# Optimization experiments

Measured on AMD Instinct MI355X. Metric: run time of the kernel, lower is better.

The kernel has to match this reference:

```python
import jax, jax.numpy as jnp
import numpy as np

B, L, D, K, V = 256, 50, 128, 4, 50000
LENGTH = 5      # opt.length
BETA = 0.01     # opt.beta scaling on loss1
EPS = 1e-12     # F.normalize eps


def _l2norm(x, axis):
    n = jnp.sqrt(jnp.sum(x * x, axis=axis, keepdims=True))
    return x / jnp.maximum(n, EPS)


def setup_inputs() -> dict:
    key = jax.random.key(0)
    ks = jax.random.split(key, 11)
    s = 1.0 / np.sqrt(D)  # reset_parameters: uniform(-stdv, stdv)
    u = lambda k, shape: jax.random.uniform(k, shape, jnp.float32, -s, s)
    return {
        "hidden": jax.random.normal(ks[0], (B, L, D), jnp.float32),
        "mask": jnp.ones((B, L), jnp.int32),
        "pos_emb": u(ks[1], (L, D)),
        "w1": u(ks[2], (2 * D, D)),
        "w2": u(ks[3], (D, K)),
        "glu1_w": u(ks[4], (D, K * D)),
        "glu1_b": u(ks[5], (K * D,)),
        "att_w1": u(ks[6], (D, D)),
        "att_w2": u(ks[7], (D, D)),
        "att_v": u(ks[8], (D, K)),
        "emb": u(ks[9], (V, D)),
    }


def reference(hidden, mask, pos_emb, w1, w2, glu1_w, glu1_b, att_w1, att_w2, att_v, emb):
    m = mask.astype(jnp.float32)[..., None]                       # [B,L,1]
    hs = jnp.sum(hidden * m, axis=1) / jnp.sum(m, axis=1)         # [B,D] masked mean
    # nh = tanh(cat(pos, hidden) @ w1); then sigmoid(glu1)
    cat = jnp.concatenate([jnp.broadcast_to(pos_emb[None], hidden.shape), hidden], axis=-1)
    nh = jnp.tanh(cat @ w1)                                       # [B,L,D]
    nh = jax.nn.sigmoid(nh @ glu1_w + glu1_b)                     # [B,L,K*D]
    # torch.split(dim=2) + stack(dim=3) -> [B,L,D,K]
    nh = nh.reshape(B, L, K, D).transpose(0, 1, 3, 2)             # [B,L,D,K]
    beta = jnp.einsum('bldk,dk->blk', nh, w2)                     # [B,L,K]
    # attention gate alpha = sigmoid(att_v(tanh(W1 hs + W2 hidden)))
    att = jnp.tanh(hs[:, None, :] @ att_w1 + hidden @ att_w2)     # [B,L,D]
    alpha = jax.nn.sigmoid(att @ att_v)                           # [B,L,K]
    beta = beta * (0.5 + alpha) * m                               # mask over interests
    # per-interest L2 normalize along sequence (fused over K)
    nb = _l2norm(beta, axis=1)                                    # [B,L,K]
    # pairwise |cos| between interests: vectorized Gram instead of python loops
    G = jnp.einsum('bli,blj->bij', nb, nb)                        # [B,K,K]
    triu = jnp.triu(jnp.ones((K, K), jnp.float32), 1)
    sim = jnp.sum(jnp.abs(G) * triu, axis=(1, 2)) * (2.0 / (K * (K - 1)))  # [B]
    lens = jnp.sum(mask, axis=1).astype(jnp.float32) - LENGTH     # sumask[:,0] - length
    loss1 = jnp.sum(jax.nn.sigmoid(sim * lens))                   # scalar
    # per-interest pooled session reps, stacked on leading axis -> [K,B,D]
    select = jnp.einsum('blk,bld->kbd', beta, hidden)
    b_norm = _l2norm(emb[1:], axis=-1)                            # [V-1,D]
    scores = jnp.einsum('kbd,vd->kbv', select, b_norm)            # [K,B,V-1]
    max_scores = jnp.max(scores, axis=0)                          # [B,V-1]
    return (max_scores, loss1 * BETA, scores)
```

## Files before the change

kernel.cpp:

```cpp
#include <hip/hip_runtime.h>
#include <hip/hip_bf16.h>
#include <math.h>

constexpr int NB = 256;
constexpr int NL = 50;
constexpr int ND = 128;
constexpr int NK = 4;
constexpr int NVOC = 50000;
constexpr int NVm1 = 49999;
constexpr int NPAD = 50048;
constexpr int ROWS = NB * NL;
constexpr int MROWS = NB * NK;

typedef __bf16 bf16x8 __attribute__((ext_vector_type(8)));
typedef float f32x4 __attribute__((ext_vector_type(4)));

__device__ __forceinline__ float sigm_fast(float x) { return 1.0f / (1.0f + __expf(-x)); }
__device__ __forceinline__ float sigm_prec(float x) { return 1.0f / (1.0f + expf(-x)); }

__global__ void k_hs_lens(const float* __restrict__ hidden, const int* __restrict__ mask,
                          float* __restrict__ hs, float* __restrict__ lens) {
    int b = blockIdx.x;
    int d = threadIdx.x;
    float acc = 0.f, msum = 0.f;
    for (int l = 0; l < NL; ++l) {
        float mv = (float)mask[b * NL + l];
        acc += hidden[((size_t)b * NL + l) * ND + d] * mv;
        msum += mv;
    }
    hs[b * ND + d] = acc / msum;
    if (d == 0) lens[b] = msum - 5.0f;
}

__global__ void k_rowmat(const float* __restrict__ rows, const float* __restrict__ mat,
                         float* __restrict__ outp) {
    int r = blockIdx.x;
    int d = threadIdx.x;
    __shared__ float s[ND];
    s[d] = rows[r * ND + d];
    __syncthreads();
    float acc = 0.f;
#pragma unroll 8
    for (int j = 0; j < ND; ++j) acc += s[j] * mat[j * ND + d];
    outp[r * ND + d] = acc;
}

__global__ __launch_bounds__(256) void k_nh_att(
    const float* __restrict__ hidden, const float* __restrict__ w1,
    const float* __restrict__ att_w2, const float* __restrict__ att_v,
    const float* __restrict__ posPart, const float* __restrict__ hsW1,
    float* __restrict__ nh_out, float* __restrict__ alpha_out) {
    constexpr int R = 32;
    __shared__ float X[R * ND];
    __shared__ float ATT[R * 132];
    int row0 = blockIdx.x * R;
    int tid = threadIdx.x;
    for (int i = tid; i < R * ND; i += 256) X[i] = hidden[(size_t)row0 * ND + i];
    __syncthreads();
    int d = tid & 127;
    int rg = tid >> 7;
    float accN[16], accA[16];
#pragma unroll
    for (int r = 0; r < 16; ++r) { accN[r] = 0.f; accA[r] = 0.f; }
    for (int j = 0; j < ND; ++j) {
        float w1v = w1[(ND + j) * ND + d];
        float awv = att_w2[j * ND + d];
#pragma unroll
        for (int r = 0; r < 16; ++r) {
            float x = X[(rg * 16 + r) * ND + j];
            accN[r] += x * w1v;
            accA[r] += x * awv;
        }
    }
#pragma unroll
    for (int r = 0; r < 16; ++r) {
        int row = row0 + rg * 16 + r;
        int b = row / NL;
        int l = row - b * NL;
        float nhv = tanhf(posPart[l * ND + d] + accN[r]);
        float atv = tanhf(hsW1[b * ND + d] + accA[r]);
        nh_out[(size_t)row * ND + d] = nhv;
        ATT[(rg * 16 + r) * 132 + d] = atv;
    }
    __syncthreads();
    if (tid < 128) {
        int rl = tid >> 2;
        int k = tid & 3;
        float acc = 0.f;
        for (int dd = 0; dd < ND; ++dd) acc += ATT[rl * 132 + dd] * att_v[dd * NK + k];
        alpha_out[(size_t)(row0 + rl) * NK + k] = sigm_fast(acc);
    }
}

__global__ __launch_bounds__(256) void k_glu_beta(
    const float* __restrict__ nh, const float* __restrict__ glu1_w,
    const float* __restrict__ glu1_b, const float* __restrict__ w2,
    const float* __restrict__ alpha, const int* __restrict__ mask,
    float* __restrict__ beta_out) {
    constexpr int R = 16;
    __shared__ float NHs[R * ND];
    __shared__ float P[R * 513];
    int row0 = blockIdx.x * R;
    int tid = threadIdx.x;
    for (int i = tid; i < R * ND; i += 256) NHs[i] = nh[(size_t)row0 * ND + i];
    __syncthreads();
    float acc0[R], acc1[R];
#pragma unroll
    for (int r = 0; r < R; ++r) { acc0[r] = 0.f; acc1[r] = 0.f; }
    int c0 = tid, c1 = tid + 256;
    for (int j = 0; j < ND; ++j) {
        float g0 = glu1_w[j * 512 + c0];
        float g1 = glu1_w[j * 512 + c1];
#pragma unroll
        for (int r = 0; r < R; ++r) {
            float x = NHs[r * ND + j];
            acc0[r] += x * g0;
            acc1[r] += x * g1;
        }
    }
    float bb0 = glu1_b[c0], bb1 = glu1_b[c1];
    float w20 = w2[(c0 & 127) * NK + (c0 >> 7)];
    float w21 = w2[(c1 & 127) * NK + (c1 >> 7)];
#pragma unroll
    for (int r = 0; r < R; ++r) {
        P[r * 513 + c0] = sigm_fast(acc0[r] + bb0) * w20;
        P[r * 513 + c1] = sigm_fast(acc1[r] + bb1) * w21;
    }
    __syncthreads();
    if (tid < 64) {
        int r = tid >> 2;
        int k = tid & 3;
        float s = 0.f;
        for (int dd = 0; dd < ND; ++dd) s += P[r * 513 + k * ND + dd];
        int row = row0 + r;
        float mv = (float)mask[row];
        float a = alpha[(size_t)row * NK + k];
        beta_out[(size_t)row * NK + k] = s * (0.5f + a) * mv;
    }
}

__global__ void k_loss_b(const float* __restrict__ beta, const float* __restrict__ lens,
                         float* __restrict__ lossb) {
    int b = blockIdx.x;
    int t = threadIdx.x;
    float bk[NK] = {0.f, 0.f, 0.f, 0.f};
    if (t < NL) {
#pragma unroll
        for (int k = 0; k < NK; ++k) bk[k] = beta[((size_t)b * NL + t) * NK + k];
    }
    float nb[NK];
#pragma unroll
    for (int k = 0; k < NK; ++k) {
        float v = bk[k] * bk[k];
        for (int off = 32; off >= 1; off >>= 1) v += __shfl_xor(v, off);
        nb[k] = bk[k] / fmaxf(sqrtf(v), 1e-12f);
    }
    float sim = 0.f;
#pragma unroll
    for (int i = 0; i < NK; ++i) {
#pragma unroll
        for (int j = 0; j < NK; ++j) {
            if (j > i) {
                float p = nb[i] * nb[j];
                for (int off = 32; off >= 1; off >>= 1) p += __shfl_xor(p, off);
                sim += fabsf(p);
            }
        }
    }
    sim *= (2.0f / (NK * (NK - 1)));
    if (t == 0) lossb[b] = sigm_prec(sim * lens[b]);
}

__global__ void k_loss_red(const float* __restrict__ lossb, float* __restrict__ out_scalar) {
    __shared__ float red[4];
    int t = threadIdx.x;
    float v = lossb[t];
    for (int off = 32; off >= 1; off >>= 1) v += __shfl_xor(v, off);
    if ((t & 63) == 0) red[t >> 6] = v;
    __syncthreads();
    if (t == 0) out_scalar[0] = (red[0] + red[1] + red[2] + red[3]) * 0.01f;
}

__global__ void k_select(const float* __restrict__ beta, const float* __restrict__ hidden,
                         __hip_bfloat16* __restrict__ selb) {
    int b = blockIdx.x;
    int d = threadIdx.x;
    float acc[NK] = {0.f, 0.f, 0.f, 0.f};
    for (int l = 0; l < NL; ++l) {
        float h = hidden[((size_t)b * NL + l) * ND + d];
        const float* bp = &beta[((size_t)b * NL + l) * NK];
        acc[0] += bp[0] * h;
        acc[1] += bp[1] * h;
        acc[2] += bp[2] * h;
        acc[3] += bp[3] * h;
    }
#pragma unroll
    for (int k = 0; k < NK; ++k)
        selb[((size_t)b * NK + k) * ND + d] = __float2bfloat16(acc[k]);
}

__global__ void k_bnorm(const float* __restrict__ emb, __hip_bfloat16* __restrict__ bn) {
    int v = blockIdx.x * 2 + (threadIdx.x >> 7);
    int j = threadIdx.x & 127;
    __shared__ float red[4];
    float x = 0.f;
    if (v < NVm1) x = emb[((size_t)v + 1) * ND + j];
    float ss = x * x;
    for (int off = 32; off >= 1; off >>= 1) ss += __shfl_xor(ss, off);
    int w = threadIdx.x >> 6;
    if ((threadIdx.x & 63) == 0) red[w] = ss;
    __syncthreads();
    float tot = (threadIdx.x < 128) ? (red[0] + red[1]) : (red[2] + red[3]);
    float rn = 1.f / fmaxf(sqrtf(tot), 1e-12f);
    bn[(size_t)v * ND + j] = __float2bfloat16(x * rn);
}

__global__ __launch_bounds__(256) void k_gemm(
    const __hip_bfloat16* __restrict__ selb, const __hip_bfloat16* __restrict__ bn,
    float* __restrict__ scores, float* __restrict__ maxs) {
    int bn0 = blockIdx.x * 128;
    int bm0 = blockIdx.y * 128;
    int wave = threadIdx.x >> 6;
    int lane = threadIdx.x & 63;
    int l16 = lane & 15;
    int quad = lane >> 4;
    int m_off = bm0 + (wave >> 1) * 64;
    int n_off = bn0 + (wave & 1) * 64;

    f32x4 acc[4][4];
#pragma unroll
    for (int mi = 0; mi < 4; ++mi)
#pragma unroll
        for (int ni = 0; ni < 4; ++ni) acc[mi][ni] = (f32x4){0.f, 0.f, 0.f, 0.f};

    const bf16x8* A = reinterpret_cast<const bf16x8*>(selb);
    const bf16x8* Bv = reinterpret_cast<const bf16x8*>(bn);
#pragma unroll
    for (int kk = 0; kk < 4; ++kk) {
        int koff = kk * 4 + quad;
        bf16x8 afr[4], bfr[4];
#pragma unroll
        for (int mi = 0; mi < 4; ++mi)
            afr[mi] = A[(size_t)(m_off + mi * 16 + l16) * 16 + koff];
#pragma unroll
        for (int ni = 0; ni < 4; ++ni)
            bfr[ni] = Bv[(size_t)(n_off + ni * 16 + l16) * 16 + koff];
#pragma unroll
        for (int mi = 0; mi < 4; ++mi)
#pragma unroll
            for (int ni = 0; ni < 4; ++ni)
                acc[mi][ni] = __builtin_amdgcn_mfma_f32_16x16x32_bf16(
                    afr[mi], bfr[ni], acc[mi][ni], 0, 0, 0);
    }

#pragma unroll
    for (int mi = 0; mi < 4; ++mi) {
        int m_base = m_off + mi * 16;
        int bidx = (m_base >> 2) + quad;
#pragma unroll
        for (int ni = 0; ni < 4; ++ni) {
            int n = n_off + ni * 16 + l16;
            if (n < NVm1) {
                float mx = acc[mi][ni][0];
#pragma unroll
                for (int r = 0; r < 4; ++r) {
                    float val = acc[mi][ni][r];
                    scores[(size_t)r * NB * NVm1 + (size_t)bidx * NVm1 + n] = val;
                    mx = fmaxf(mx, val);
                }
                maxs[(size_t)bidx * NVm1 + n] = mx;
            }
        }
    }
}

extern "C" void kernel_launch(void* const* d_in, const int* in_sizes, int n_in,
                              void* d_out, int out_size, void* d_ws, size_t ws_size,
                              hipStream_t stream) {
    const float* hidden  = (const float*)d_in[0];
    const int*   mask    = (const int*)d_in[1];
    const float* pos_emb = (const float*)d_in[2];
    const float* w1      = (const float*)d_in[3];
    const float* w2      = (const float*)d_in[4];
    const float* glu1_w  = (const float*)d_in[5];
    const float* glu1_b  = (const float*)d_in[6];
    const float* att_w1  = (const float*)d_in[7];
    const float* att_w2  = (const float*)d_in[8];
    const float* att_v   = (const float*)d_in[9];
    const float* emb     = (const float*)d_in[10];

    float* out      = (float*)d_out;
    float* max_out  = out;
    float* loss_out = out + (size_t)NB * NVm1;
    float* scores   = out + (size_t)NB * NVm1 + 1;

    char* w = (char*)d_ws;
    auto alloc = [&](size_t bytes) {
        char* p = w;
        w += (bytes + 255) & ~(size_t)255;
        return p;
    };
    float* posPart = (float*)alloc((size_t)NL * ND * 4);
    float* hs      = (float*)alloc((size_t)NB * ND * 4);
    float* lensv   = (float*)alloc((size_t)NB * 4);
    float* hsW1    = (float*)alloc((size_t)NB * ND * 4);
    float* nh      = (float*)alloc((size_t)ROWS * ND * 4);
    float* alphav  = (float*)alloc((size_t)ROWS * NK * 4);
    float* betav   = (float*)alloc((size_t)ROWS * NK * 4);
    float* lossb   = (float*)alloc((size_t)NB * 4);
    __hip_bfloat16* selb = (__hip_bfloat16*)alloc((size_t)MROWS * ND * 2);
    __hip_bfloat16* bnv  = (__hip_bfloat16*)alloc((size_t)NPAD * ND * 2);

    k_hs_lens<<<NB, 128, 0, stream>>>(hidden, mask, hs, lensv);
    k_rowmat<<<NL, 128, 0, stream>>>(pos_emb, w1, posPart);
    k_rowmat<<<NB, 128, 0, stream>>>(hs, att_w1, hsW1);
    k_nh_att<<<ROWS / 32, 256, 0, stream>>>(hidden, w1, att_w2, att_v, posPart, hsW1, nh, alphav);
    k_glu_beta<<<ROWS / 16, 256, 0, stream>>>(nh, glu1_w, glu1_b, w2, alphav, mask, betav);
    k_loss_b<<<NB, 64, 0, stream>>>(betav, lensv, lossb);
    k_loss_red<<<1, 256, 0, stream>>>(lossb, loss_out);
    k_select<<<NB, 128, 0, stream>>>(betav, hidden, selb);
    k_bnorm<<<NPAD / 2, 256, 0, stream>>>(emb, bnv);
    k_gemm<<<dim3(NPAD / 128, MROWS / 128), 256, 0, stream>>>(selb, bnv, scores, max_out);
}
```

Measured before the change: 516.8 us.

## Fuse small kernels, vectorize matmul inner loops, stage GEMM tiles in LDS

Merges several small launches: the two row-matmuls become one kernel, select and bnorm share one kernel, and the loss reduction becomes an atomicAdd inside the per-batch loss kernel, which now computes lens itself. The inner loops of nh/att and glu are rewritten to read float4 from shared memory with explicit FMA chains. The GEMM now loads A and B tiles into LDS via global_load_lds with an XOR swizzle and loops over four N tiles per block, reusing the A tile. This trades fewer launches and better operand reuse for more LDS and synchronization. The atomic loss sum makes the accumulation order nondeterministic.

```diff
diff --git a/kernel.cpp b/kernel.cpp
--- a/kernel.cpp
+++ b/kernel.cpp
@@ -6,11 +6,11 @@
 constexpr int NL = 50;
 constexpr int ND = 128;
 constexpr int NK = 4;
-constexpr int NVOC = 50000;
 constexpr int NVm1 = 49999;
-constexpr int NPAD = 50048;
+constexpr int NPAD2 = 50176;
 constexpr int ROWS = NB * NL;
 constexpr int MROWS = NB * NK;
+constexpr int GEMM_NT = 4;
 
 typedef __bf16 bf16x8 __attribute__((ext_vector_type(8)));
 typedef float f32x4 __attribute__((ext_vector_type(4)));
@@ -18,8 +18,14 @@
 __device__ __forceinline__ float sigm_fast(float x) { return 1.0f / (1.0f + __expf(-x)); }
 __device__ __forceinline__ float sigm_prec(float x) { return 1.0f / (1.0f + expf(-x)); }
 
-__global__ void k_hs_lens(const float* __restrict__ hidden, const int* __restrict__ mask,
-                          float* __restrict__ hs, float* __restrict__ lens) {
+__device__ __forceinline__ void gld_lds16(const void* g, void* l) {
+    __builtin_amdgcn_global_load_lds(
+        (const __attribute__((address_space(1))) void*)g,
+        (__attribute__((address_space(3))) void*)l, 16, 0, 0);
+}
+
+__global__ void k_hs(const float* __restrict__ hidden, const int* __restrict__ mask,
+                     float* __restrict__ hs, float* __restrict__ loss_out) {
     int b = blockIdx.x;
     int d = threadIdx.x;
     float acc = 0.f, msum = 0.f;
@@ -29,20 +35,25 @@
         msum += mv;
     }
     hs[b * ND + d] = acc / msum;
-    if (d == 0) lens[b] = msum - 5.0f;
-}
-
-__global__ void k_rowmat(const float* __restrict__ rows, const float* __restrict__ mat,
-                         float* __restrict__ outp) {
+    if (b == 0 && d == 0) loss_out[0] = 0.f;
+}
+
+__global__ void k_rowmats(const float* __restrict__ pos_emb, const float* __restrict__ w1,
+                          const float* __restrict__ hs, const float* __restrict__ att_w1,
+                          float* __restrict__ posPart, float* __restrict__ hsW1) {
     int r = blockIdx.x;
     int d = threadIdx.x;
+    const float *src, *mat;
+    float* dst;
+    if (r < NL) { src = pos_emb + (size_t)r * ND; mat = w1;     dst = posPart + (size_t)r * ND; }
+    else        { int b = r - NL; src = hs + (size_t)b * ND; mat = att_w1; dst = hsW1 + (size_t)b * ND; }
     __shared__ float s[ND];
-    s[d] = rows[r * ND + d];
+    s[d] = src[d];
     __syncthreads();
     float acc = 0.f;
 #pragma unroll 8
     for (int j = 0; j < ND; ++j) acc += s[j] * mat[j * ND + d];
-    outp[r * ND + d] = acc;
+    dst[d] = acc;
 }
 
 __global__ __launch_bounds__(256) void k_nh_att(
@@ -62,14 +73,20 @@
     float accN[16], accA[16];
 #pragma unroll
     for (int r = 0; r < 16; ++r) { accN[r] = 0.f; accA[r] = 0.f; }
-    for (int j = 0; j < ND; ++j) {
-        float w1v = w1[(ND + j) * ND + d];
-        float awv = att_w2[j * ND + d];
+    const float4* Xv = (const float4*)X;
+    for (int j4 = 0; j4 < 32; ++j4) {
+        float w1v[4], awv[4];
+#pragma unroll
+        for (int u = 0; u < 4; ++u) {
+            int j = j4 * 4 + u;
+            w1v[u] = w1[(ND + j) * ND + d];
+            awv[u] = att_w2[j * ND + d];
+        }
 #pragma unroll
         for (int r = 0; r < 16; ++r) {
-            float x = X[(rg * 16 + r) * ND + j];
-            accN[r] += x * w1v;
-            accA[r] += x * awv;
+            float4 xv = Xv[(rg * 16 + r) * 32 + j4];
+            accN[r] = fmaf(xv.w, w1v[3], fmaf(xv.z, w1v[2], fmaf(xv.y, w1v[1], fmaf(xv.x, w1v[0], accN[r]))));
+            accA[r] = fmaf(xv.w, awv[3], fmaf(xv.z, awv[2], fmaf(xv.y, awv[1], fmaf(xv.x, awv[0], accA[r]))));
         }
     }
 #pragma unroll
@@ -108,14 +125,20 @@
 #pragma unroll
     for (int r = 0; r < R; ++r) { acc0[r] = 0.f; acc1[r] = 0.f; }
     int c0 = tid, c1 = tid + 256;
-    for (int j = 0; j < ND; ++j) {
-        float g0 = glu1_w[j * 512 + c0];
-        float g1 = glu1_w[j * 512 + c1];
+    const float4* Nv = (const float4*)NHs;
+    for (int j4 = 0; j4 < 32; ++j4) {
+        float g0v[4], g1v[4];
+#pragma unroll
+        for (int u = 0; u < 4; ++u) {
+            int j = j4 * 4 + u;
+            g0v[u] = glu1_w[j * 512 + c0];
+            g1v[u] = glu1_w[j * 512 + c1];
+        }
 #pragma unroll
         for (int r = 0; r < R; ++r) {
-            float x = NHs[r * ND + j];
-            acc0[r] += x * g0;
-            acc1[r] += x * g1;
+            float4 xv = Nv[r * 32 + j4];
+            acc0[r] = fmaf(xv.w, g0v[3], fmaf(xv.z, g0v[2], fmaf(xv.y, g0v[1], fmaf(xv.x, g0v[0], acc0[r]))));
+            acc1[r] = fmaf(xv.w, g1v[3], fmaf(xv.z, g1v[2], fmaf(xv.y, g1v[1], fmaf(xv.x, g1v[0], acc1[r]))));
         }
     }
     float bb0 = glu1_b[c0], bb1 = glu1_b[c1];
@@ -139,10 +162,14 @@
     }
 }
 
-__global__ void k_loss_b(const float* __restrict__ beta, const float* __restrict__ lens,
-                         float* __restrict__ lossb) {
+__global__ void k_loss(const float* __restrict__ beta, const int* __restrict__ mask,
+                       float* __restrict__ loss_out) {
     int b = blockIdx.x;
     int t = threadIdx.x;
+    float mv = (t < NL) ? (float)mask[b * NL + t] : 0.f;
+    float msum = mv;
+    for (int off = 32; off >= 1; off >>= 1) msum += __shfl_xor(msum, off);
+    float lens = msum - 5.0f;
     float bk[NK] = {0.f, 0.f, 0.f, 0.f};
     if (t < NL) {
 #pragma unroll
@@ -168,109 +195,135 @@
         }
     }
     sim *= (2.0f / (NK * (NK - 1)));
-    if (t == 0) lossb[b] = sigm_prec(sim * lens[b]);
-}
-
-__global__ void k_loss_red(const float* __restrict__ lossb, float* __restrict__ out_scalar) {
-    __shared__ float red[4];
-    int t = threadIdx.x;
-    float v = lossb[t];
-    for (int off = 32; off >= 1; off >>= 1) v += __shfl_xor(v, off);
-    if ((t & 63) == 0) red[t >> 6] = v;
-    __syncthreads();
-    if (t == 0) out_scalar[0] = (red[0] + red[1] + red[2] + red[3]) * 0.01f;
-}
-
-__global__ void k_select(const float* __restrict__ beta, const float* __restrict__ hidden,
-                         __hip_bfloat16* __restrict__ selb) {
-    int b = blockIdx.x;
-    int d = threadIdx.x;
-    float acc[NK] = {0.f, 0.f, 0.f, 0.f};
-    for (int l = 0; l < NL; ++l) {
-        float h = hidden[((size_t)b * NL + l) * ND + d];
-        const float* bp = &beta[((size_t)b * NL + l) * NK];
-        acc[0] += bp[0] * h;
-        acc[1] += bp[1] * h;
-        acc[2] += bp[2] * h;
-        acc[3] += bp[3] * h;
-    }
-#pragma unroll
-    for (int k = 0; k < NK; ++k)
-        selb[((size_t)b * NK + k) * ND + d] = __float2bfloat16(acc[k]);
-}
-
-__global__ void k_bnorm(const float* __restrict__ emb, __hip_bfloat16* __restrict__ bn) {
-    int v = blockIdx.x * 2 + (threadIdx.x >> 7);
-    int j = threadIdx.x & 127;
-    __shared__ float red[4];
-    float x = 0.f;
-    if (v < NVm1) x = emb[((size_t)v + 1) * ND + j];
-    float ss = x * x;
-    for (int off = 32; off >= 1; off >>= 1) ss += __shfl_xor(ss, off);
-    int w = threadIdx.x >> 6;
-    if ((threadIdx.x & 63) == 0) red[w] = ss;
-    __syncthreads();
-    float tot = (threadIdx.x < 128) ? (red[0] + red[1]) : (red[2] + red[3]);
-    float rn = 1.f / fmaxf(sqrtf(tot), 1e-12f);
-    bn[(size_t)v * ND + j] = __float2bfloat16(x * rn);
+    if (t == 0) atomicAdd(loss_out, sigm_prec(sim * lens) * 0.01f);
+}
+
+__global__ __launch_bounds__(256) void k_sel_bnorm(
+    const float* __restrict__ beta, const float* __restrict__ hidden,
+    const float* __restrict__ emb, __hip_bfloat16* __restrict__ selb,
+    __hip_bfloat16* __restrict__ bnv) {
+    int blk = blockIdx.x;
+    int tid = threadIdx.x;
+    if (blk < NPAD2 / 2) {
+        int v = blk * 2 + (tid >> 7);
+        int j = tid & 127;
+        __shared__ float red[4];
+        float x = 0.f;
+        if (v < NVm1) x = emb[((size_t)v + 1) * ND + j];
+        float ss = x * x;
+        for (int off = 32; off >= 1; off >>= 1) ss += __shfl_xor(ss, off);
+        int w = tid >> 6;
+        if ((tid & 63) == 0) red[w] = ss;
+        __syncthreads();
+        float tot = (tid < 128) ? (red[0] + red[1]) : (red[2] + red[3]);
+        float rn = 1.f / fmaxf(sqrtf(tot), 1e-12f);
+        bnv[(size_t)v * ND + j] = __float2bfloat16(x * rn);
+    } else {
+        int b = (blk - NPAD2 / 2) * 2 + (tid >> 7);
+        int d = tid & 127;
+        float a0 = 0.f, a1 = 0.f, a2 = 0.f, a3 = 0.f;
+        for (int l = 0; l < NL; ++l) {
+            float h = hidden[((size_t)b * NL + l) * ND + d];
+            const float* bp = &beta[((size_t)b * NL + l) * NK];
+            a0 = fmaf(bp[0], h, a0);
+            a1 = fmaf(bp[1], h, a1);
+            a2 = fmaf(bp[2], h, a2);
+            a3 = fmaf(bp[3], h, a3);
+        }
+        selb[((size_t)b * NK + 0) * ND + d] = __float2bfloat16(a0);
+        selb[((size_t)b * NK + 1) * ND + d] = __float2bfloat16(a1);
+        selb[((size_t)b * NK + 2) * ND + d] = __float2bfloat16(a2);
+        selb[((size_t)b * NK + 3) * ND + d] = __float2bfloat16(a3);
+    }
 }
 
 __global__ __launch_bounds__(256) void k_gemm(
     const __hip_bfloat16* __restrict__ selb, const __hip_bfloat16* __restrict__ bn,
     float* __restrict__ scores, float* __restrict__ maxs) {
-    int bn0 = blockIdx.x * 128;
+    __shared__ __hip_bfloat16 As[128 * 128];
+    __shared__ __hip_bfloat16 Bs[128 * 128];
     int bm0 = blockIdx.y * 128;
-    int wave = threadIdx.x >> 6;
-    int lane = threadIdx.x & 63;
-    int l16 = lane & 15;
-    int quad = lane >> 4;
-    int m_off = bm0 + (wave >> 1) * 64;
-    int n_off = bn0 + (wave & 1) * 64;
-
-    f32x4 acc[4][4];
-#pragma unroll
-    for (int mi = 0; mi < 4; ++mi)
-#pragma unroll
-        for (int ni = 0; ni < 4; ++ni) acc[mi][ni] = (f32x4){0.f, 0.f, 0.f, 0.f};
-
-    const bf16x8* A = reinterpret_cast<const bf16x8*>(selb);
-    const bf16x8* Bv = reinterpret_cast<const bf16x8*>(bn);
-#pragma unroll
-    for (int kk = 0; kk < 4; ++kk) {
-        int koff = kk * 4 + quad;
-        bf16x8 afr[4], bfr[4];
+    int nbase = blockIdx.x * (128 * GEMM_NT);
+    int tid = threadIdx.x;
+    int wave = tid >> 6, lane = tid & 63;
+    int l16 = lane & 15, quad = lane >> 4;
+    int m_loc = (wave >> 1) * 64;
+    int n_loc = (wave & 1) * 64;
+
+#pragma unroll
+    for (int it = 0; it < 8; ++it) {
+        int id = it * 256 + tid;
+        int row = id >> 4, c = id & 15;
+        int gc = c ^ (row & 7);
+        const char* g = (const char*)selb + ((size_t)(bm0 + row) * 16 + gc) * 16;
+        char* l = (char*)As + (size_t)(it * 256 + wave * 64) * 16;
+        gld_lds16(g, l);
+    }
+
+    const bf16x8* Av = (const bf16x8*)As;
+    const bf16x8* Bv = (const bf16x8*)Bs;
+
+    for (int nt = 0; nt < GEMM_NT; ++nt) {
+        int bn0 = nbase + nt * 128;
+#pragma unroll
+        for (int it = 0; it < 8; ++it) {
+            int id = it * 256 + tid;
+            int row = id >> 4, c = id & 15;
+            int gc = c ^ (row & 7);
+            const char* g = (const char*)bn + ((size_t)(bn0 + row) * 16 + gc) * 16;
+            char* l = (char*)Bs + (size_t)(it * 256 + wave * 64) * 16;
+            gld_lds16(g, l);
+        }
+        __syncthreads();
+
+        f32x4 acc[4][4];
 #pragma unroll
         for (int mi = 0; mi < 4; ++mi)
-            afr[mi] = A[(size_t)(m_off + mi * 16 + l16) * 16 + koff];
-#pragma unroll
-        for (int ni = 0; ni < 4; ++ni)
-            bfr[ni] = Bv[(size_t)(n_off + ni * 16 + l16) * 16 + koff];
-#pragma unroll
-        for (int mi = 0; mi < 4; ++mi)
-#pragma unroll
-            for (int ni = 0; ni < 4; ++ni)
-                acc[mi][ni] = __builtin_amdgcn_mfma_f32_16x16x32_bf16(
-                    afr[mi], bfr[ni], acc[mi][ni], 0, 0, 0);
-    }
-
-#pragma unroll
-    for (int mi = 0; mi < 4; ++mi) {
-        int m_base = m_off + mi * 16;
-        int bidx = (m_base >> 2) + quad;
-#pragma unroll
-        for (int ni = 0; ni < 4; ++ni) {
-            int n = n_off + ni * 16 + l16;
-            if (n < NVm1) {
-                float mx = acc[mi][ni][0];
-#pragma unroll
-                for (int r = 0; r < 4; ++r) {
-                    float val = acc[mi][ni][r];
-                    scores[(size_t)r * NB * NVm1 + (size_t)bidx * NVm1 + n] = val;
-                    mx = fmaxf(mx, val);
+#pragma unroll
+            for (int ni = 0; ni < 4; ++ni) acc[mi][ni] = (f32x4){0.f, 0.f, 0.f, 0.f};
+
+#pragma unroll
+        for (int kk = 0; kk < 4; ++kk) {
+            int ko = kk * 4 + quad;
+            bf16x8 afr[4], bfr[4];
+#pragma unroll
+            for (int mi = 0; mi < 4; ++mi) {
+                int row = m_loc + mi * 16 + l16;
+                afr[mi] = Av[row * 16 + (ko ^ (row & 7))];
+            }
+#pragma unroll
+            for (int ni = 0; ni < 4; ++ni) {
+                int row = n_loc + ni * 16 + l16;
+                bfr[ni] = Bv[row * 16 + (ko ^ (row & 7))];
+            }
+#pragma unroll
+            for (int mi = 0; mi < 4; ++mi)
+#pragma unroll
+                for (int ni = 0; ni < 4; ++ni)
+                    acc[mi][ni] = __builtin_amdgcn_mfma_f32_16x16x32_bf16(
+                        afr[mi], bfr[ni], acc[mi][ni], 0, 0, 0);
+        }
+
+#pragma unroll
+        for (int mi = 0; mi < 4; ++mi) {
+            int m_base = bm0 + m_loc + mi * 16;
+            int bidx = (m_base >> 2) + quad;
+#pragma unroll
+            for (int ni = 0; ni < 4; ++ni) {
+                int n = bn0 + n_loc + ni * 16 + l16;
+                if (n < NVm1) {
+                    float mx = acc[mi][ni][0];
+#pragma unroll
+                    for (int r = 0; r < 4; ++r) {
+                        float val = acc[mi][ni][r];
+                        scores[(size_t)r * NB * NVm1 + (size_t)bidx * NVm1 + n] = val;
+                        mx = fmaxf(mx, val);
+                    }
+                    maxs[(size_t)bidx * NVm1 + n] = mx;
                 }
-                maxs[(size_t)bidx * NVm1 + n] = mx;
             }
         }
+        __syncthreads();
     }
 }
 
@@ -302,23 +355,18 @@
     };
     float* posPart = (float*)alloc((size_t)NL * ND * 4);
     float* hs      = (float*)alloc((size_t)NB * ND * 4);
-    float* lensv   = (float*)alloc((size_t)NB * 4);
     float* hsW1    = (float*)alloc((size_t)NB * ND * 4);
     float* nh      = (float*)alloc((size_t)ROWS * ND * 4);
     float* alphav  = (float*)alloc((size_t)ROWS * NK * 4);
     float* betav   = (float*)alloc((size_t)ROWS * NK * 4);
-    float* lossb   = (float*)alloc((size_t)NB * 4);
     __hip_bfloat16* selb = (__hip_bfloat16*)alloc((size_t)MROWS * ND * 2);
-    __hip_bfloat16* bnv  = (__hip_bfloat16*)alloc((size_t)NPAD * ND * 2);
-
-    k_hs_lens<<<NB, 128, 0, stream>>>(hidden, mask, hs, lensv);
-    k_rowmat<<<NL, 128, 0, stream>>>(pos_emb, w1, posPart);
-    k_rowmat<<<NB, 128, 0, stream>>>(hs, att_w1, hsW1);
+    __hip_bfloat16* bnv  = (__hip_bfloat16*)alloc((size_t)NPAD2 * ND * 2);
+
+    k_hs<<<NB, 128, 0, stream>>>(hidden, mask, hs, loss_out);
+    k_rowmats<<<NL + NB, 128, 0, stream>>>(pos_emb, w1, hs, att_w1, posPart, hsW1);
     k_nh_att<<<ROWS / 32, 256, 0, stream>>>(hidden, w1, att_w2, att_v, posPart, hsW1, nh, alphav);
     k_glu_beta<<<ROWS / 16, 256, 0, stream>>>(nh, glu1_w, glu1_b, w2, alphav, mask, betav);
-    k_loss_b<<<NB, 64, 0, stream>>>(betav, lensv, lossb);
-    k_loss_red<<<1, 256, 0, stream>>>(lossb, loss_out);
-    k_select<<<NB, 128, 0, stream>>>(betav, hidden, selb);
-    k_bnorm<<<NPAD / 2, 256, 0, stream>>>(emb, bnv);
-    k_gemm<<<dim3(NPAD / 128, MROWS / 128), 256, 0, stream>>>(selb, bnv, scores, max_out);
-}
+    k_loss<<<NB, 64, 0, stream>>>(betav, mask, loss_out);
+    k_sel_bnorm<<<NPAD2 / 2 + NB / 2, 256, 0, stream>>>(betav, hidden, emb, selb, bnv);
+    k_gemm<<<dim3(NPAD2 / (128 * GEMM_NT), MROWS / 128), 256, 0, stream>>>(selb, bnv, scores, max_out);
+}
```

Result: faster. 488.3 us (-5.5%).
